# Optimization experiments

Measured on AMD Instinct MI355X. Metric: run time of the kernel, lower is better.

Reference implementation:

```python
import jax, jax.numpy as jnp
import numpy as np

DIM = 384
DEPTH = 4
HEADS = 6
DIM_HEAD = 64
INNER = HEADS * DIM_HEAD  # 384
MLP = 1536
B, N = 4, 2048


def setup_inputs() -> dict:
    key = jax.random.key(0)
    ks = jax.random.split(key, 7)
    s = 0.02
    x = jax.random.normal(ks[0], (B, N, DIM), dtype=jnp.float32)
    Wqkv = jax.random.normal(ks[1], (DEPTH, DIM, 3 * INNER), dtype=jnp.float32) * s
    Wout = jax.random.normal(ks[2], (DEPTH, INNER, DIM), dtype=jnp.float32) * s
    W1 = jax.random.normal(ks[3], (DEPTH, DIM, MLP), dtype=jnp.float32) * s
    b1 = jax.random.normal(ks[4], (DEPTH, MLP), dtype=jnp.float32) * s
    W2 = jax.random.normal(ks[5], (DEPTH, MLP, DIM), dtype=jnp.float32) * s
    b2 = jax.random.normal(ks[6], (DEPTH, DIM), dtype=jnp.float32) * s
    return {"x": x, "Wqkv": Wqkv, "Wout": Wout, "W1": W1, "b1": b1, "W2": W2, "b2": b2}


def _attention(x, Wqkv_l, Wout_l):
    scale = DIM_HEAD ** (-0.5)
    qkv = jnp.einsum('bnd,de->bne', x, Wqkv_l)  # [B,N,3*INNER]
    q, k, v = jnp.split(qkv, 3, axis=-1)
    # [B,N,INNER] -> [B,H,N,Dh]
    reshape = lambda t: t.reshape(B, N, HEADS, DIM_HEAD).transpose(0, 2, 1, 3)
    q, k, v = reshape(q), reshape(k), reshape(v)
    dots = jnp.einsum('bhnd,bhmd->bhnm', q, k) * scale
    attn = jax.nn.softmax(dots, axis=-1)
    out = jnp.einsum('bhnm,bhmd->bhnd', attn, v)
    out = out.transpose(0, 2, 1, 3).reshape(B, N, INNER)
    return jnp.einsum('bne,ed->bnd', out, Wout_l)


def _ff(x, W1_l, b1_l, W2_l, b2_l):
    h = jax.nn.gelu(jnp.einsum('bnd,dh->bnh', x, W1_l) + b1_l, approximate=False)
    return jnp.einsum('bnh,hd->bnd', h, W2_l) + b2_l


def reference(x, Wqkv, Wout, W1, b1, W2, b2):
    for l in range(DEPTH):
        x = _attention(x, Wqkv[l], Wout[l]) + x
        x = _ff(x, W1[l], b1[l], W2[l], b2[l]) + x
    return x
```

## Files before the change

### kernel.cpp

```cpp
#include <hip/hip_runtime.h>
#include <stdint.h>

#define HEADS 6
#define NN 2048
#define BB 4
#define MTOT (BB*NN)
#define DEPTH 4

typedef unsigned short u16;
typedef __attribute__((ext_vector_type(8))) short bf16x8;
typedef __attribute__((ext_vector_type(4))) float f32x4;
typedef __attribute__((ext_vector_type(16))) float f32x16;

#define MFMA32(a,b,c) __builtin_amdgcn_mfma_f32_32x32x16_bf16((a),(b),(c),0,0,0)

#define QSC 0.18033688011112042f

__device__ __forceinline__ u16 f2bf(float f) {
  union { float f; uint32_t u; } v; v.f = f;
  uint32_t r = v.u + 0x7fffu + ((v.u >> 16) & 1u);
  return (u16)(r >> 16);
}

__device__ __forceinline__ uint32_t pk2(float lo, float hi) {
  uint32_t r;
  asm("v_cvt_pk_bf16_f32 %0, %1, %2" : "=v"(r) : "v"(lo), "v"(hi));
  return r;
}

__device__ __forceinline__ void gload_lds16(const void* g, void* l) {
  __builtin_amdgcn_global_load_lds((const __attribute__((address_space(1))) void*)g,
                                   (__attribute__((address_space(3))) void*)l, 16, 0, 0);
}

__global__ __launch_bounds__(256)
void wtrans_k(const float* __restrict__ in, u16* __restrict__ out, int K, int N) {
  __shared__ float t[32][33];
  const int z = blockIdx.z;
  in  += (size_t)z * K * N;
  out += (size_t)z * K * N;
  const int n0 = blockIdx.x * 32, k0 = blockIdx.y * 32;
  const int tx = threadIdx.x & 31, ty = threadIdx.x >> 5;
#pragma unroll
  for (int i = 0; i < 4; ++i)
    t[ty + i*8][tx] = in[(size_t)(k0 + ty + i*8) * N + n0 + tx];
  __syncthreads();
#pragma unroll
  for (int i = 0; i < 4; ++i)
    out[(size_t)(n0 + ty + i*8) * K + k0 + tx] = f2bf(t[tx][ty + i*8]);
}

__global__ __launch_bounds__(256)
void xprep_k(const float* __restrict__ x, u16* __restrict__ xbf, int n) {
  int i = blockIdx.x * 256 + threadIdx.x;
  if (i < n) xbf[i] = f2bf(x[i]);
}

template<int MODE>
__global__ __launch_bounds__(256)
void gemm64_k(const u16* __restrict__ A, const u16* __restrict__ Bt,
              const float* __restrict__ bias, const float* __restrict__ res,
              float* __restrict__ outF, u16* __restrict__ outB,
              u16* __restrict__ qb, u16* __restrict__ kb, u16* __restrict__ vtb,
              int M, int N, int K) {
  __shared__ u16 smA[64 * 64];
  __shared__ u16 smB[64 * 64];
  const int tid = threadIdx.x;
  const int lane = tid & 63, wv = tid >> 6;
  const int wr = wv >> 1, wc = wv & 1;
  const int l31 = lane & 31, h2 = lane >> 5;
  const int row0 = blockIdx.y * 64, col0 = blockIdx.x * 64;

  f32x16 acc;
#pragma unroll
  for (int i = 0; i < 16; ++i) acc[i] = 0.f;

  const int c0 = tid, c1 = tid + 256;
  const int r0 = c0 >> 3, s0 = (c0 & 7) ^ (r0 & 7);
  const int r1 = c1 >> 3, s1 = (c1 & 7) ^ (r1 & 7);

  const int ksteps = K >> 6;
  for (int kt = 0; kt < ksteps; ++kt) {
    const int k0 = kt << 6;
    const u16* Ab = A  + (size_t)row0 * K + k0;
    const u16* Bb = Bt + (size_t)col0 * K + k0;
    gload_lds16(Ab + (size_t)r0 * K + s0 * 8, smA + wv * 512);
    gload_lds16(Ab + (size_t)r1 * K + s1 * 8, smA + 2048 + wv * 512);
    gload_lds16(Bb + (size_t)r0 * K + s0 * 8, smB + wv * 512);
    gload_lds16(Bb + (size_t)r1 * K + s1 * 8, smB + 2048 + wv * 512);
    __syncthreads();
    const int ra = wr * 32 + l31;
    const int rb = wc * 32 + l31;
#pragma unroll
    for (int ks = 0; ks < 4; ++ks) {
      bf16x8 af = *(const bf16x8*)(smA + ra * 64 + (((ks * 2 + h2) ^ (ra & 7)) * 8));
      bf16x8 bf = *(const bf16x8*)(smB + rb * 64 + (((ks * 2 + h2) ^ (rb & 7)) * 8));
      acc = MFMA32(af, bf, acc);
    }
    __syncthreads();
  }

  const int col = col0 + wc * 32 + l31;
  if (MODE == 0) {
    const int sec = col / 384, c3 = col - sec * 384;
    const int hh = c3 >> 6, d = c3 & 63;
#pragma unroll
    for (int c = 0; c < 4; ++c)
#pragma unroll
      for (int j = 0; j < 4; ++j) {
        const int row = row0 + wr * 32 + 8 * c + 4 * h2 + j;
        const int bb = row >> 11, n = row & 2047;
        const float v = acc[4 * c + j];
        if (sec == 0)       qb [(((size_t)bb * HEADS + hh) * NN + n) * 64 + d] = f2bf(v * QSC);
        else if (sec == 1)  kb [(((size_t)bb * HEADS + hh) * NN + n) * 64 + d] = f2bf(v);
        else                vtb[(((size_t)bb * HEADS + hh) * 64 + d) * NN + n] = f2bf(v);
      }
  } else {
#pragma unroll
    for (int c = 0; c < 4; ++c)
#pragma unroll
      for (int j = 0; j < 4; ++j) {
        const int row = row0 + wr * 32 + 8 * c + 4 * h2 + j;
        float v = acc[4 * c + j];
        if (MODE == 1) {
          size_t idx = (size_t)row * N + col;
          v += res[idx];
          outF[idx] = v;
          outB[idx] = f2bf(v);
        } else if (MODE == 2) {
          v += bias[col];
          v = 0.5f * v * (1.0f + erff(v * 0.70710678118f));
          outB[(size_t)row * N + col] = f2bf(v);
        } else {
          size_t idx = (size_t)row * N + col;
          v += bias[col] + res[idx];
          outF[idx] = v;
          outB[idx] = f2bf(v);
        }
      }
  }
}

__global__ __launch_bounds__(256)
void attn_k(const u16* __restrict__ qb, const u16* __restrict__ kb,
            const u16* __restrict__ vtb, u16* __restrict__ ob) {
  __shared__ u16 kb3[3][2][32 * 64];
  __shared__ u16 vb3[3][2][64 * 32];
  const int tid = threadIdx.x;
  const int lane = tid & 63, wv = tid >> 6;
  const int l31 = lane & 31, h2 = lane >> 5;
  const int hs = wv >> 1;
  const int qg = wv & 1;

  const int lid = blockIdx.y * 32 + blockIdx.x;
  const int xcd = lid & 7, ii = lid >> 3;
  const int bh = 3 * xcd + (ii >> 5);
  const int qblk = ii & 31;
  const int b = bh / HEADS, h = bh - b * HEADS;
  const int q0 = qblk * 64 + qg * 32;

  const u16* Qb = qb + ((size_t)bh * NN + q0 + l31) * 64;
  bf16x8 qf[4];
#pragma unroll
  for (int ct2 = 0; ct2 < 4; ++ct2)
    qf[ct2] = *(const bf16x8*)(Qb + ct2 * 16 + h2 * 8);

  float m = -1e30f, s = 0.f;
  f32x16 acc[2];
#pragma unroll
  for (int dg = 0; dg < 2; ++dg)
#pragma unroll
    for (int i = 0; i < 16; ++i) acc[dg][i] = 0.f;
  const f32x16 zero16 = {0.f,0.f,0.f,0.f,0.f,0.f,0.f,0.f,0.f,0.f,0.f,0.f,0.f,0.f,0.f,0.f};

  const u16* Kb0 = kb  + (size_t)bh * NN * 64;
  const u16* Vt0 = vtb + (size_t)bh * 64 * NN;
  const int rK = tid >> 3, sK = (tid & 7) ^ (rK & 7);
  const int rV = tid >> 2, sV = (tid & 3) ^ (rV & 3);

#define STAGE3(kd, vd, t) do { \
    _Pragma("unroll") \
    for (int hf = 0; hf < 2; ++hf) { \
      gload_lds16(Kb0 + ((size_t)(hf * 1024 + (t) * 32 + rK)) * 64 + sK * 8, \
                  (kd) + hf * 2048 + wv * 512); \
      gload_lds16(Vt0 + (size_t)rV * NN + hf * 1024 + (t) * 32 + sV * 8, \
                  (vd) + hf * 2048 + wv * 512); \
    } \
  } while (0)

  u16 *kA = &kb3[0][0][0], *kB = &kb3[1][0][0], *kC = &kb3[2][0][0];
  u16 *vA = &vb3[0][0][0], *vB = &vb3[1][0][0], *vC = &vb3[2][0][0];

  STAGE3(kA, vA, 0);
  __syncthreads();

  bf16x8 pf[2];
  const int NT = 1024 / 32;
  for (int kt = 0; kt < NT; ++kt) {
    if (kt + 1 < NT) STAGE3(kB, vB, kt + 1);

    f32x16 st = zero16;
    {
      const u16* krow = kA + hs * 2048 + l31 * 64;
#pragma unroll
      for (int ct2 = 0; ct2 < 4; ++ct2) {
        bf16x8 kf = *(const bf16x8*)(krow + (((ct2 * 2 + h2) ^ (l31 & 7)) * 8));
        st = MFMA32(kf, qf[ct2], st);
      }
    }
    if (kt > 0) {
#pragma unroll
      for (int ks = 0; ks < 2; ++ks)
#pragma unroll
        for (int dg = 0; dg < 2; ++dg) {
          const int d = dg * 32 + l31;
          bf16x8 vf = *(const bf16x8*)(vC + hs * 2048 + d * 32 + (((ks * 2 + h2) ^ (d & 3)) * 8));
          acc[dg] = MFMA32(vf, pf[ks], acc[dg]);
        }
    }

    float tmax = -1e30f;
#pragma unroll
    for (int i = 0; i < 16; ++i) tmax = fmaxf(tmax, st[i]);
    if (!__all(tmax <= m + 8.0f)) {
      float rm = fmaxf(tmax, __shfl_xor(tmax, 32));
      float mn = fmaxf(m, rm);
      float al = __builtin_amdgcn_exp2f(m - mn);
      s *= al;
#pragma unroll
      for (int dg = 0; dg < 2; ++dg)
#pragma unroll
        for (int i = 0; i < 16; ++i) acc[dg][i] *= al;
      m = mn;
    }
    float p[16];
    float r = 0.f;
#pragma unroll
    for (int i = 0; i < 16; ++i) {
      float t = __builtin_amdgcn_exp2f(st[i] - m);
      p[i] = t;
      r += t;
    }
    r += __shfl_xor(r, 32);
    s += r;

#pragma unroll
    for (int sub = 0; sub < 2; ++sub) {
      const int s8 = sub * 8;
      uint32_t X0 = pk2(p[s8 + 0], p[s8 + 1]);
      uint32_t X1 = pk2(p[s8 + 2], p[s8 + 3]);
      uint32_t Y0 = pk2(p[s8 + 4], p[s8 + 5]);
      uint32_t Y1 = pk2(p[s8 + 6], p[s8 + 7]);
      asm volatile("v_permlane32_swap_b32 %0, %1" : "+v"(X0), "+v"(Y0));
      asm volatile("v_permlane32_swap_b32 %0, %1" : "+v"(X1), "+v"(Y1));
      union { uint32_t u[4]; bf16x8 v; } pu;
      pu.u[0] = X0; pu.u[1] = X1; pu.u[2] = Y0; pu.u[3] = Y1;
      pf[sub] = pu.v;
    }

    __syncthreads();
    u16* t1 = kA; kA = kB; kB = kC; kC = t1;
    u16* t2 = vA; vA = vB; vB = vC; vC = t2;
  }

#pragma unroll
  for (int ks = 0; ks < 2; ++ks)
#pragma unroll
    for (int dg = 0; dg < 2; ++dg) {
      const int d = dg * 32 + l31;
      bf16x8 vf = *(const bf16x8*)(vC + hs * 2048 + d * 32 + (((ks * 2 + h2) ^ (d & 3)) * 8));
      acc[dg] = MFMA32(vf, pf[ks], acc[dg]);
    }

  float* mb = (float*)kb3;
  if (wv >= 2) {
    const int base = ((wv - 2) * 64 + lane) * 36;
#pragma unroll
    for (int dg = 0; dg < 2; ++dg)
#pragma unroll
      for (int i = 0; i < 16; ++i) mb[base + dg * 16 + i] = acc[dg][i];
    mb[base + 32] = m;
    mb[base + 33] = s;
  }
  __syncthreads();
  if (wv < 2) {
    const int base = (wv * 64 + lane) * 36;
    const float m2 = mb[base + 32], s2 = mb[base + 33];
    const float M  = fmaxf(m, m2);
    const float a1 = __builtin_amdgcn_exp2f(m  - M);
    const float a2 = __builtin_amdgcn_exp2f(m2 - M);
    const float inv = 1.f / (s * a1 + s2 * a2);
    u16* orow = ob + ((size_t)b * NN + q0 + l31) * 384 + h * 64;
#pragma unroll
    for (int dg = 0; dg < 2; ++dg)
#pragma unroll
      for (int c = 0; c < 4; ++c) {
        float v0 = (acc[dg][4*c + 0] * a1 + mb[base + dg*16 + 4*c + 0] * a2) * inv;
        float v1 = (acc[dg][4*c + 1] * a1 + mb[base + dg*16 + 4*c + 1] * a2) * inv;
        float v2 = (acc[dg][4*c + 2] * a1 + mb[base + dg*16 + 4*c + 2] * a2) * inv;
        float v3 = (acc[dg][4*c + 3] * a1 + mb[base + dg*16 + 4*c + 3] * a2) * inv;
        uint2 w;
        w.x = pk2(v0, v1);
        w.y = pk2(v2, v3);
        *(uint2*)(orow + dg * 32 + 8 * c + 4 * h2) = w;
      }
  }
}

extern "C" void kernel_launch(void* const* d_in, const int* in_sizes, int n_in,
                              void* d_out, int out_size, void* d_ws, size_t ws_size,
                              hipStream_t stream) {
  (void)in_sizes; (void)n_in; (void)out_size; (void)ws_size;
  const float* x    = (const float*)d_in[0];
  const float* Wqkv = (const float*)d_in[1];
  const float* Wout = (const float*)d_in[2];
  const float* W1   = (const float*)d_in[3];
  const float* b1   = (const float*)d_in[4];
  const float* W2   = (const float*)d_in[5];
  const float* b2   = (const float*)d_in[6];
  float* out = (float*)d_out;

  char* ws = (char*)d_ws;
  size_t off = 0;
  auto alloc = [&](size_t bytes) { char* p = ws + off; off += (bytes + 255) & ~(size_t)255; return p; };
  u16*   wqkvT = (u16*)alloc((size_t)DEPTH * 1152 * 384 * 2);
  u16*   woutT = (u16*)alloc((size_t)DEPTH * 384 * 384 * 2);
  u16*   w1T   = (u16*)alloc((size_t)DEPTH * 1536 * 384 * 2);
  u16*   w2T   = (u16*)alloc((size_t)DEPTH * 384 * 1536 * 2);
  u16*   xbf   = (u16*)alloc((size_t)MTOT * 384 * 2);
  float* xres  = (float*)alloc((size_t)MTOT * 384 * 4);
  u16*   qbuf  = (u16*)alloc((size_t)MTOT * 384 * 2);
  u16*   kbuf  = (u16*)alloc((size_t)MTOT * 384 * 2);
  u16*   vtbuf = (u16*)alloc((size_t)MTOT * 384 * 2);
  u16*   obuf  = (u16*)alloc((size_t)MTOT * 384 * 2);
  u16*   hbuf  = (u16*)alloc((size_t)MTOT * 1536 * 2);

  wtrans_k<<<dim3(1152/32, 384/32, DEPTH), 256, 0, stream>>>(Wqkv, wqkvT, 384, 1152);
  wtrans_k<<<dim3( 384/32, 384/32, DEPTH), 256, 0, stream>>>(Wout, woutT, 384, 384);
  wtrans_k<<<dim3(1536/32, 384/32, DEPTH), 256, 0, stream>>>(W1,   w1T,   384, 1536);
  wtrans_k<<<dim3( 384/32,1536/32, DEPTH), 256, 0, stream>>>(W2,   w2T,   1536, 384);
  xprep_k<<<(MTOT*384 + 255)/256, 256, 0, stream>>>(x, xbf, MTOT*384);

  for (int l = 0; l < DEPTH; ++l) {
    gemm64_k<0><<<dim3(1152/64, MTOT/64), 256, 0, stream>>>(
        xbf, wqkvT + (size_t)l*1152*384, nullptr, nullptr, nullptr, nullptr,
        qbuf, kbuf, vtbuf, MTOT, 1152, 384);
    attn_k<<<dim3(32, 24), 256, 0, stream>>>(qbuf, kbuf, vtbuf, obuf);
    gemm64_k<1><<<dim3(384/64, MTOT/64), 256, 0, stream>>>(
        obuf, woutT + (size_t)l*384*384, nullptr, (l == 0 ? x : xres), xres, xbf,
        nullptr, nullptr, nullptr, MTOT, 384, 384);
    gemm64_k<2><<<dim3(1536/64, MTOT/64), 256, 0, stream>>>(
        xbf, w1T + (size_t)l*1536*384, b1 + l*1536, nullptr, nullptr, hbuf,
        nullptr, nullptr, nullptr, MTOT, 1536, 384);
    gemm64_k<3><<<dim3(384/64, MTOT/64), 256, 0, stream>>>(
        hbuf, w2T + (size_t)l*384*1536, b2 + l*384, xres,
        (l == DEPTH-1 ? out : xres), xbf,
        nullptr, nullptr, nullptr, MTOT, 384, 1536);
  }
}
```

Measured before the change: 539.4 us.

## Replace triple-buffered skewed attention pipeline with plain double buffering

The attention kernel drops its three-stage K/V ring buffer, where the PV matmul for the previous tile was deferred and overlapped with the current QK matmul. It now uses two LDS buffers and does the PV MFMAs on the current tile right after the softmax. This cuts LDS use and removes the epilogue PV step, which may improve occupancy. The cost is the loss of overlap between softmax and MFMA work across iterations.

```diff
diff --git a/kernel.cpp b/kernel.cpp
--- a/kernel.cpp
+++ b/kernel.cpp
@@ -144,8 +144,7 @@
 __global__ __launch_bounds__(256)
 void attn_k(const u16* __restrict__ qb, const u16* __restrict__ kb,
             const u16* __restrict__ vtb, u16* __restrict__ ob) {
-  __shared__ u16 kb3[3][2][32 * 64];
-  __shared__ u16 vb3[3][2][64 * 32];
+  __shared__ u16 sall[4][4096];
   const int tid = threadIdx.x;
   const int lane = tid & 63, wv = tid >> 6;
   const int l31 = lane & 31, h2 = lane >> 5;
@@ -178,45 +177,34 @@
   const int rK = tid >> 3, sK = (tid & 7) ^ (rK & 7);
   const int rV = tid >> 2, sV = (tid & 3) ^ (rV & 3);
 
-#define STAGE3(kd, vd, t) do { \
+#define STAGE2(buf, t) do { \
     _Pragma("unroll") \
     for (int hf = 0; hf < 2; ++hf) { \
       gload_lds16(Kb0 + ((size_t)(hf * 1024 + (t) * 32 + rK)) * 64 + sK * 8, \
-                  (kd) + hf * 2048 + wv * 512); \
+                  sall[buf] + hf * 2048 + wv * 512); \
       gload_lds16(Vt0 + (size_t)rV * NN + hf * 1024 + (t) * 32 + sV * 8, \
-                  (vd) + hf * 2048 + wv * 512); \
+                  sall[2 + (buf)] + hf * 2048 + wv * 512); \
     } \
   } while (0)
 
-  u16 *kA = &kb3[0][0][0], *kB = &kb3[1][0][0], *kC = &kb3[2][0][0];
-  u16 *vA = &vb3[0][0][0], *vB = &vb3[1][0][0], *vC = &vb3[2][0][0];
-
-  STAGE3(kA, vA, 0);
+  STAGE2(0, 0);
   __syncthreads();
 
-  bf16x8 pf[2];
+  int cur = 0;
   const int NT = 1024 / 32;
   for (int kt = 0; kt < NT; ++kt) {
-    if (kt + 1 < NT) STAGE3(kB, vB, kt + 1);
+    if (kt + 1 < NT) STAGE2(cur ^ 1, kt + 1);
+    const u16* kcur = sall[cur] + hs * 2048;
+    const u16* vcur = sall[2 + cur] + hs * 2048;
 
     f32x16 st = zero16;
     {
-      const u16* krow = kA + hs * 2048 + l31 * 64;
+      const u16* krow = kcur + l31 * 64;
 #pragma unroll
       for (int ct2 = 0; ct2 < 4; ++ct2) {
         bf16x8 kf = *(const bf16x8*)(krow + (((ct2 * 2 + h2) ^ (l31 & 7)) * 8));
         st = MFMA32(kf, qf[ct2], st);
       }
-    }
-    if (kt > 0) {
-#pragma unroll
-      for (int ks = 0; ks < 2; ++ks)
-#pragma unroll
-        for (int dg = 0; dg < 2; ++dg) {
-          const int d = dg * 32 + l31;
-          bf16x8 vf = *(const bf16x8*)(vC + hs * 2048 + d * 32 + (((ks * 2 + h2) ^ (d & 3)) * 8));
-          acc[dg] = MFMA32(vf, pf[ks], acc[dg]);
-        }
     }
 
     float tmax = -1e30f;
@@ -244,6 +232,7 @@
     r += __shfl_xor(r, 32);
     s += r;
 
+    bf16x8 pf[2];
 #pragma unroll
     for (int sub = 0; sub < 2; ++sub) {
       const int s8 = sub * 8;
@@ -258,21 +247,20 @@
       pf[sub] = pu.v;
     }
 
+#pragma unroll
+    for (int ks = 0; ks < 2; ++ks)
+#pragma unroll
+      for (int dg = 0; dg < 2; ++dg) {
+        const int d = dg * 32 + l31;
+        bf16x8 vf = *(const bf16x8*)(vcur + d * 32 + (((ks * 2 + h2) ^ (d & 3)) * 8));
+        acc[dg] = MFMA32(vf, pf[ks], acc[dg]);
+      }
+
     __syncthreads();
-    u16* t1 = kA; kA = kB; kB = kC; kC = t1;
-    u16* t2 = vA; vA = vB; vB = vC; vC = t2;
-  }
-
-#pragma unroll
-  for (int ks = 0; ks < 2; ++ks)
-#pragma unroll
-    for (int dg = 0; dg < 2; ++dg) {
-      const int d = dg * 32 + l31;
-      bf16x8 vf = *(const bf16x8*)(vC + hs * 2048 + d * 32 + (((ks * 2 + h2) ^ (d & 3)) * 8));
-      acc[dg] = MFMA32(vf, pf[ks], acc[dg]);
-    }
-
-  float* mb = (float*)kb3;
+    cur ^= 1;
+  }
+
+  float* mb = (float*)sall;
   if (wv >= 2) {
     const int base = ((wv - 2) * 64 + lane) * 36;
 #pragma unroll
```

New measurement: 555.7 us. 1.03x slower.
